# Performance work log

Hardware: AMD Instinct MI355X
Metric: run time of the kernel (lower is better)

The kernel has to match this reference:

```python
import jax, jax.numpy as jnp
import numpy as np

B, A, D = 512, 32, 256      # batch clips, actors (nodes per graph), feature dim
E = 1048576                 # total edges over the flattened (B*A)-node graph
THRESHOLD = 0.5             # config.knn.threshold
EPS = 1e-5


def setup_inputs() -> dict:
    key = jax.random.key(0)
    k1, k2, k3 = jax.random.split(key, 3)
    N = B * A
    X = jax.random.normal(k1, (B, A, D), dtype=jnp.float32)
    edge_index = jax.random.randint(k2, (2, E), 0, N, dtype=jnp.int32)
    W = jax.random.normal(k3, (D, D), dtype=jnp.float32) * (1.0 / np.sqrt(D))
    b = jnp.zeros((D,), dtype=jnp.float32)
    return {"X": X, "edge_index": edge_index, "W": W, "b": b}


def gcn_conv(x, edge_index, W, b):
    # Standard GCNConv: x' = D^-1/2 (A + I) D^-1/2 (x W) + b
    N = x.shape[0]
    x = x @ W                                            # [N, D]
    loop = jnp.arange(N, dtype=edge_index.dtype)
    src = jnp.concatenate([edge_index[0], loop])         # message sources
    tgt = jnp.concatenate([edge_index[1], loop])         # aggregation targets
    deg = jax.ops.segment_sum(jnp.ones_like(src, dtype=x.dtype), tgt,
                              num_segments=N)            # in-degree incl. self-loop
    dinv = jnp.where(deg > 0, jax.lax.rsqrt(deg), 0.0)
    coef = (dinv[src] * dinv[tgt])[:, None]              # symmetric norm per edge
    out = jax.ops.segment_sum(x[src] * coef, tgt, num_segments=N)
    return out + b


def reference(X, edge_index, W, b):
    Bq, Aq, Dq = X.shape
    x = X.reshape(Bq * Aq, Dq)
    x = gcn_conv(x, edge_index, W, b)
    Xo = x.reshape(Bq, Aq, Dq)

    # cal_edge: pairwise squared distances per batch, min-max normalized,
    # thresholded. Instead of variable-length dense_to_sparse edge lists we
    # return the equivalent fixed-shape adjacency mask [B, A, A].
    inner = -2.0 * jnp.einsum('bad,bcd->bac', Xo, Xo)
    sq = jnp.sum(Xo * Xo, axis=-1, keepdims=True)        # [B, A, 1]
    scores = sq + inner + jnp.swapaxes(sq, -1, -2)       # [B, A, A]
    smin = scores.min(axis=-1, keepdims=True)
    smax = scores.max(axis=-1, keepdims=True)
    scores = (scores - smin) / (smax - smin + EPS)
    adj_mask = scores > THRESHOLD                        # new edge set (dense form)
    return Xo, adj_mask
```

## Files before the change

### kernel.cpp

```cpp
#include <hip/hip_runtime.h>

#define BQ 512
#define AQ 32
#define DQ 256
#define NQ (BQ * AQ)
#define EQ 1048576
#define THR 0.5f
#define EPSF 1e-5f
#define DEG_STRIDE 160
#define BIN_TGTS 64
#define NBINS (NQ / BIN_TGTS)
#define BIN_STRIDE 4864

typedef __attribute__((ext_vector_type(8))) short bf16x8;
typedef __attribute__((ext_vector_type(4))) float f32x4;

__device__ __forceinline__ unsigned short f2bf(float f) {
    unsigned int u = __float_as_uint(f);
    return (unsigned short)((u + 0x7FFFu + ((u >> 16) & 1u)) >> 16);
}
__device__ __forceinline__ float bf2f(unsigned short h) {
    return __uint_as_float((unsigned int)h << 16);
}

__global__ __launch_bounds__(256) void k_prep_part(
        const float* __restrict__ W, unsigned short* __restrict__ Wt,
        const int* __restrict__ src, const int* __restrict__ tgt,
        int* __restrict__ bin_cursor, unsigned int* __restrict__ binned) {
    __shared__ int hist[NBINS];
    int tid = threadIdx.x;
    if (blockIdx.x < 256) {
        int idx = blockIdx.x * 256 + tid;
        int n = idx >> 8;
        int k = idx & 255;
        float w = W[k * DQ + n];
        unsigned short h = f2bf(w);
        Wt[idx] = h;
        Wt[DQ * DQ + idx] = f2bf(w - bf2f(h));
        return;
    }
    hist[tid] = 0;
    __syncthreads();
    int base = (blockIdx.x - 256) * 4096;
    int t[16], s[16];
    #pragma unroll
    for (int i = 0; i < 16; i++) {
        int e = base + i * 256 + tid;
        t[i] = tgt[e];
        s[i] = src[e];
        atomicAdd(&hist[t[i] >> 6], 1);
    }
    __syncthreads();
    int mine = hist[tid];
    __syncthreads();
    hist[tid] = tid * BIN_STRIDE + atomicAdd(&bin_cursor[tid], mine);
    __syncthreads();
    #pragma unroll
    for (int i = 0; i < 16; i++) {
        int slot = atomicAdd(&hist[t[i] >> 6], 1);
        binned[slot] = ((unsigned int)t[i] << 14) | (unsigned int)s[i];
    }
}

__global__ __launch_bounds__(256) void k_bucket_gemm(
        const float* __restrict__ Xp, const unsigned short* __restrict__ Wt,
        unsigned short* __restrict__ xwb,
        const int* __restrict__ bin_cursor, const unsigned int* __restrict__ binned,
        unsigned short* __restrict__ bucket, int* __restrict__ cnt,
        float* __restrict__ dinv) {
    __shared__ unsigned short lbuck[BIN_TGTS * DEG_STRIDE];
    __shared__ int lcnt[BIN_TGTS];
    int tid = threadIdx.x;
    if (blockIdx.x < NBINS) {
        int b = blockIdx.x;
        if (tid < BIN_TGTS) lcnt[tid] = 0;
        __syncthreads();
        int beg = b * BIN_STRIDE;
        int count = bin_cursor[b];
        if (count > BIN_STRIDE) count = BIN_STRIDE;
        int end = beg + count;
        for (int i = beg + tid; i < end; i += 256) {
            unsigned int ed = binned[i];
            int tl = (int)(ed >> 14) & 63;
            int pos = atomicAdd(&lcnt[tl], 1);
            if (pos < DEG_STRIDE)
                lbuck[tl * DEG_STRIDE + pos] = (unsigned short)(ed & 0x3FFFu);
        }
        __syncthreads();
        const unsigned int* lb32 = (const unsigned int*)lbuck;
        unsigned int* gb32 = (unsigned int*)(bucket + (size_t)b * BIN_TGTS * DEG_STRIDE);
        #pragma unroll
        for (int i = 0; i < 20; i++) gb32[i * 256 + tid] = lb32[i * 256 + tid];
        if (tid < BIN_TGTS) {
            int c = lcnt[tid];
            cnt[b * BIN_TGTS + tid] = c;
            dinv[b * BIN_TGTS + tid] = rsqrtf((float)(c + 1));
        }
        return;
    }
    int wave = tid >> 6;
    int lane = tid & 63;
    int col = lane & 15;
    int quad = lane >> 4;
    int mbase = (blockIdx.x - NBINS) * 64 + wave * 16;
    int m = mbase + col;

    const float* arow = Xp + (size_t)m * DQ;
    const unsigned short* Wlo = Wt + DQ * DQ;

    f32x4 acc[16];
    f32x4 zero = {0.f, 0.f, 0.f, 0.f};
    #pragma unroll
    for (int i = 0; i < 16; i++) acc[i] = zero;

    for (int k0 = 0; k0 < DQ; k0 += 32) {
        int kq = k0 + quad * 8;
        float4 a0 = *(const float4*)(arow + kq);
        float4 a1 = *(const float4*)(arow + kq + 4);
        float av[8] = {a0.x, a0.y, a0.z, a0.w, a1.x, a1.y, a1.z, a1.w};
        bf16x8 ah, al;
        #pragma unroll
        for (int j = 0; j < 8; j++) {
            unsigned short h = f2bf(av[j]);
            ah[j] = (short)h;
            al[j] = (short)f2bf(av[j] - bf2f(h));
        }
        #pragma unroll
        for (int nt = 0; nt < 16; nt++) {
            size_t boff = (size_t)(nt * 16 + col) * DQ + kq;
            bf16x8 bh = *(const bf16x8*)(Wt + boff);
            bf16x8 bl = *(const bf16x8*)(Wlo + boff);
            acc[nt] = __builtin_amdgcn_mfma_f32_16x16x32_bf16(ah, bh, acc[nt], 0, 0, 0);
            acc[nt] = __builtin_amdgcn_mfma_f32_16x16x32_bf16(al, bh, acc[nt], 0, 0, 0);
            acc[nt] = __builtin_amdgcn_mfma_f32_16x16x32_bf16(ah, bl, acc[nt], 0, 0, 0);
        }
    }

    #pragma unroll
    for (int nt = 0; nt < 16; nt++) {
        #pragma unroll
        for (int r = 0; r < 4; r++) {
            xwb[(size_t)(mbase + quad * 4 + r) * DQ + nt * 16 + col] =
                f2bf(acc[nt][r]);
        }
    }
}

__global__ __launch_bounds__(256) void k_agg(const unsigned int* __restrict__ xwb,
                                             const int* __restrict__ cnt,
                                             const unsigned short* __restrict__ bucket,
                                             const float* __restrict__ dinv,
                                             const float* __restrict__ bias,
                                             float* __restrict__ out) {
    int wave = threadIdx.x >> 6;
    int lane = threadIdx.x & 63;
    int t = blockIdx.x * 4 + wave;
    const uint2* xw2 = (const uint2*)xwb;

    float dt = dinv[t];
    float c0 = dt * dt;
    uint2 sp = xw2[(size_t)t * 64 + lane];
    float4 acc;
    acc.x = __uint_as_float(sp.x << 16) * c0;
    acc.y = __uint_as_float(sp.x & 0xFFFF0000u) * c0;
    acc.z = __uint_as_float(sp.y << 16) * c0;
    acc.w = __uint_as_float(sp.y & 0xFFFF0000u) * c0;

    const unsigned short* brow = bucket + t * DEG_STRIDE;
    int num = cnt[t];
    if (num > DEG_STRIDE) num = DEG_STRIDE;
    for (int k0 = 0; k0 < num; k0 += 64) {
        int rem = num - k0;
        int n = rem < 64 ? rem : 64;
        int idx = k0 + (lane < n ? lane : 0);
        int e = (int)brow[idx];
        float cl = (lane < n) ? dinv[e] * dt : 0.f;
        int n8 = (n + 7) & ~7;
        for (int j0 = 0; j0 < n8; j0 += 8) {
            #pragma unroll
            for (int jj = 0; jj < 8; jj++) {
                int j = j0 + jj;
                int s = __shfl(e, j);
                float c = __shfl(cl, j);
                uint2 p = xw2[(size_t)s * 64 + lane];
                acc.x += __uint_as_float(p.x << 16) * c;
                acc.y += __uint_as_float(p.x & 0xFFFF0000u) * c;
                acc.z += __uint_as_float(p.y << 16) * c;
                acc.w += __uint_as_float(p.y & 0xFFFF0000u) * c;
            }
        }
    }

    float4 bv = ((const float4*)bias)[lane];
    acc.x += bv.x; acc.y += bv.y; acc.z += bv.z; acc.w += bv.w;
    ((float4*)out)[(size_t)t * 64 + lane] = acc;
}

__global__ __launch_bounds__(256) void k_scores(const float* __restrict__ xo,
                                                float* __restrict__ mask) {
    __shared__ float xs[AQ][DQ + 4];
    __shared__ float sq[AQ];
    __shared__ float sc[AQ][AQ + 1];
    __shared__ float rmin[AQ], rmax[AQ];

    int bq = blockIdx.x;
    int tid = threadIdx.x;
    const float* xb = xo + (size_t)bq * AQ * DQ;

    #pragma unroll
    for (int k = 0; k < 8; k++) {
        int fidx = k * 256 + tid;
        float4 v = ((const float4*)xb)[fidx];
        *(float4*)&xs[fidx >> 6][(fidx & 63) * 4] = v;
    }
    __syncthreads();

    if (tid < AQ) {
        const float4* xi = (const float4*)xs[tid];
        float s = 0.f;
        #pragma unroll 8
        for (int dd = 0; dd < DQ / 4; dd++) {
            float4 a = xi[dd];
            s += a.x * a.x + a.y * a.y + a.z * a.z + a.w * a.w;
        }
        sq[tid] = s;
    }
    __syncthreads();

    {
        int p0 = tid * 4;
        int i = p0 >> 5;
        int j0 = p0 & 31;
        const float4* xi = (const float4*)xs[i];
        float g[4] = {0.f, 0.f, 0.f, 0.f};
        for (int dd = 0; dd < DQ / 4; dd += 8) {
            float4 ar[8];
            #pragma unroll
            for (int u = 0; u < 8; u++) ar[u] = xi[dd + u];
            #pragma unroll
            for (int q = 0; q < 4; q++) {
                const float4* xj = (const float4*)xs[j0 + q];
                float gq = 0.f;
                #pragma unroll
                for (int u = 0; u < 8; u++) {
                    float4 b = xj[dd + u];
                    gq += ar[u].x * b.x + ar[u].y * b.y +
                          ar[u].z * b.z + ar[u].w * b.w;
                }
                g[q] += gq;
            }
        }
        #pragma unroll
        for (int q = 0; q < 4; q++) {
            sc[i][j0 + q] = sq[i] - 2.f * g[q] + sq[j0 + q];
        }
    }
    __syncthreads();

    if (tid < AQ) {
        float mn = sc[tid][0], mx = sc[tid][0];
        for (int j = 1; j < AQ; j++) {
            float v = sc[tid][j];
            mn = fminf(mn, v);
            mx = fmaxf(mx, v);
        }
        rmin[tid] = mn;
        rmax[tid] = mx;
    }
    __syncthreads();

    float* mb = mask + (size_t)bq * AQ * AQ;
    {
        int p0 = tid * 4;
        int i = p0 >> 5, j0 = p0 & 31;
        float inv = 1.0f / (rmax[i] - rmin[i] + EPSF);
        float4 mv;
        mv.x = ((sc[i][j0 + 0] - rmin[i]) * inv > THR) ? 1.0f : 0.0f;
        mv.y = ((sc[i][j0 + 1] - rmin[i]) * inv > THR) ? 1.0f : 0.0f;
        mv.z = ((sc[i][j0 + 2] - rmin[i]) * inv > THR) ? 1.0f : 0.0f;
        mv.w = ((sc[i][j0 + 3] - rmin[i]) * inv > THR) ? 1.0f : 0.0f;
        ((float4*)mb)[tid] = mv;
    }
}

extern "C" void kernel_launch(void* const* d_in, const int* in_sizes, int n_in,
                              void* d_out, int out_size, void* d_ws, size_t ws_size,
                              hipStream_t stream) {
    const float* X    = (const float*)d_in[0];
    const int*   ei   = (const int*)d_in[1];
    const float* W    = (const float*)d_in[2];
    const float* bias = (const float*)d_in[3];
    float* out = (float*)d_out;

    char* ws = (char*)d_ws;
    unsigned short* xwb = (unsigned short*)ws;
    unsigned short* bucket = (unsigned short*)(ws + (size_t)NQ * DQ * 2);
    unsigned int* binned = (unsigned int*)(bucket + (size_t)NQ * DEG_STRIDE);
    unsigned short* Wt = (unsigned short*)(binned + (size_t)NBINS * BIN_STRIDE);
    int* cnt = (int*)(Wt + 2 * DQ * DQ);
    float* dinv = (float*)(cnt + NQ);
    int* bin_cursor = (int*)(dinv + NQ);

    const int* src = ei;
    const int* tgt = ei + EQ;

    hipMemsetAsync(bin_cursor, 0, NBINS * sizeof(int), stream);
    k_prep_part<<<512, 256, 0, stream>>>(W, Wt, src, tgt, bin_cursor, binned);
    k_bucket_gemm<<<512, 256, 0, stream>>>(X, Wt, xwb, bin_cursor, binned,
                                           bucket, cnt, dinv);
    k_agg<<<NQ / 4, 256, 0, stream>>>((const unsigned int*)xwb, cnt, bucket,
                                      dinv, bias, out);
    k_scores<<<BQ, 256, 0, stream>>>(out, out + (size_t)NQ * DQ);
}
```

Before: 190.3 us.

## Fuse edge aggregation and pairwise score kernels into one per-batch block

Merges the aggregation kernel and the score/mask kernel into a single launch with one 512-thread block per batch clip. Each of the 8 waves aggregates 4 actors and writes the result both to global output and directly into shared memory, so the score stage no longer re-reads the output from global memory and one launch is removed. The trade-off is fewer, larger blocks (512 instead of 4096 blocks for aggregation), which reduces the parallelism available to hide the latency of the irregular gather loads.

```diff
diff --git a/kernel.cpp b/kernel.cpp
--- a/kernel.cpp
+++ b/kernel.cpp
@@ -146,72 +146,68 @@
     }
 }
 
-__global__ __launch_bounds__(256) void k_agg(const unsigned int* __restrict__ xwb,
-                                             const int* __restrict__ cnt,
-                                             const unsigned short* __restrict__ bucket,
-                                             const float* __restrict__ dinv,
-                                             const float* __restrict__ bias,
-                                             float* __restrict__ out) {
-    int wave = threadIdx.x >> 6;
-    int lane = threadIdx.x & 63;
-    int t = blockIdx.x * 4 + wave;
-    const uint2* xw2 = (const uint2*)xwb;
-
-    float dt = dinv[t];
-    float c0 = dt * dt;
-    uint2 sp = xw2[(size_t)t * 64 + lane];
-    float4 acc;
-    acc.x = __uint_as_float(sp.x << 16) * c0;
-    acc.y = __uint_as_float(sp.x & 0xFFFF0000u) * c0;
-    acc.z = __uint_as_float(sp.y << 16) * c0;
-    acc.w = __uint_as_float(sp.y & 0xFFFF0000u) * c0;
-
-    const unsigned short* brow = bucket + t * DEG_STRIDE;
-    int num = cnt[t];
-    if (num > DEG_STRIDE) num = DEG_STRIDE;
-    for (int k0 = 0; k0 < num; k0 += 64) {
-        int rem = num - k0;
-        int n = rem < 64 ? rem : 64;
-        int idx = k0 + (lane < n ? lane : 0);
-        int e = (int)brow[idx];
-        float cl = (lane < n) ? dinv[e] * dt : 0.f;
-        int n8 = (n + 7) & ~7;
-        for (int j0 = 0; j0 < n8; j0 += 8) {
-            #pragma unroll
-            for (int jj = 0; jj < 8; jj++) {
-                int j = j0 + jj;
-                int s = __shfl(e, j);
-                float c = __shfl(cl, j);
-                uint2 p = xw2[(size_t)s * 64 + lane];
-                acc.x += __uint_as_float(p.x << 16) * c;
-                acc.y += __uint_as_float(p.x & 0xFFFF0000u) * c;
-                acc.z += __uint_as_float(p.y << 16) * c;
-                acc.w += __uint_as_float(p.y & 0xFFFF0000u) * c;
-            }
-        }
-    }
-
-    float4 bv = ((const float4*)bias)[lane];
-    acc.x += bv.x; acc.y += bv.y; acc.z += bv.z; acc.w += bv.w;
-    ((float4*)out)[(size_t)t * 64 + lane] = acc;
-}
-
-__global__ __launch_bounds__(256) void k_scores(const float* __restrict__ xo,
-                                                float* __restrict__ mask) {
+__global__ __launch_bounds__(512) void k_agg_scores(
+        const unsigned int* __restrict__ xwb,
+        const int* __restrict__ cnt,
+        const unsigned short* __restrict__ bucket,
+        const float* __restrict__ dinv,
+        const float* __restrict__ bias,
+        float* __restrict__ out,
+        float* __restrict__ mask) {
     __shared__ float xs[AQ][DQ + 4];
     __shared__ float sq[AQ];
     __shared__ float sc[AQ][AQ + 1];
     __shared__ float rmin[AQ], rmax[AQ];
 
+    int tid = threadIdx.x;
+    int wave = tid >> 6;
+    int lane = tid & 63;
     int bq = blockIdx.x;
-    int tid = threadIdx.x;
-    const float* xb = xo + (size_t)bq * AQ * DQ;
-
-    #pragma unroll
-    for (int k = 0; k < 8; k++) {
-        int fidx = k * 256 + tid;
-        float4 v = ((const float4*)xb)[fidx];
-        *(float4*)&xs[fidx >> 6][(fidx & 63) * 4] = v;
+    const uint2* xw2 = (const uint2*)xwb;
+
+    float4 bv = ((const float4*)bias)[lane];
+
+    #pragma unroll 1
+    for (int i = 0; i < 4; i++) {
+        int a = wave * 4 + i;
+        int t = bq * AQ + a;
+        float dt = dinv[t];
+        float c0 = dt * dt;
+        uint2 sp = xw2[(size_t)t * 64 + lane];
+        float4 acc;
+        acc.x = __uint_as_float(sp.x << 16) * c0;
+        acc.y = __uint_as_float(sp.x & 0xFFFF0000u) * c0;
+        acc.z = __uint_as_float(sp.y << 16) * c0;
+        acc.w = __uint_as_float(sp.y & 0xFFFF0000u) * c0;
+
+        const unsigned short* brow = bucket + t * DEG_STRIDE;
+        int num = cnt[t];
+        if (num > DEG_STRIDE) num = DEG_STRIDE;
+        for (int k0 = 0; k0 < num; k0 += 64) {
+            int rem = num - k0;
+            int n = rem < 64 ? rem : 64;
+            int idx = k0 + (lane < n ? lane : 0);
+            int e = (int)brow[idx];
+            float cl = (lane < n) ? dinv[e] * dt : 0.f;
+            int n8 = (n + 7) & ~7;
+            for (int j0 = 0; j0 < n8; j0 += 8) {
+                #pragma unroll
+                for (int jj = 0; jj < 8; jj++) {
+                    int j = j0 + jj;
+                    int s = __shfl(e, j);
+                    float c = __shfl(cl, j);
+                    uint2 p = xw2[(size_t)s * 64 + lane];
+                    acc.x += __uint_as_float(p.x << 16) * c;
+                    acc.y += __uint_as_float(p.x & 0xFFFF0000u) * c;
+                    acc.z += __uint_as_float(p.y << 16) * c;
+                    acc.w += __uint_as_float(p.y & 0xFFFF0000u) * c;
+                }
+            }
+        }
+
+        acc.x += bv.x; acc.y += bv.y; acc.z += bv.z; acc.w += bv.w;
+        ((float4*)out)[(size_t)t * 64 + lane] = acc;
+        *(float4*)&xs[a][lane * 4] = acc;
     }
     __syncthreads();
 
@@ -228,17 +224,17 @@
     __syncthreads();
 
     {
-        int p0 = tid * 4;
+        int p0 = tid * 2;
         int i = p0 >> 5;
         int j0 = p0 & 31;
         const float4* xi = (const float4*)xs[i];
-        float g[4] = {0.f, 0.f, 0.f, 0.f};
+        float g[2] = {0.f, 0.f};
         for (int dd = 0; dd < DQ / 4; dd += 8) {
             float4 ar[8];
             #pragma unroll
             for (int u = 0; u < 8; u++) ar[u] = xi[dd + u];
             #pragma unroll
-            for (int q = 0; q < 4; q++) {
+            for (int q = 0; q < 2; q++) {
                 const float4* xj = (const float4*)xs[j0 + q];
                 float gq = 0.f;
                 #pragma unroll
@@ -251,7 +247,7 @@
             }
         }
         #pragma unroll
-        for (int q = 0; q < 4; q++) {
+        for (int q = 0; q < 2; q++) {
             sc[i][j0 + q] = sq[i] - 2.f * g[q] + sq[j0 + q];
         }
     }
@@ -269,17 +265,15 @@
     }
     __syncthreads();
 
-    float* mb = mask + (size_t)bq * AQ * AQ;
     {
-        int p0 = tid * 4;
+        float* mb = mask + (size_t)bq * AQ * AQ;
+        int p0 = tid * 2;
         int i = p0 >> 5, j0 = p0 & 31;
         float inv = 1.0f / (rmax[i] - rmin[i] + EPSF);
-        float4 mv;
+        float2 mv;
         mv.x = ((sc[i][j0 + 0] - rmin[i]) * inv > THR) ? 1.0f : 0.0f;
         mv.y = ((sc[i][j0 + 1] - rmin[i]) * inv > THR) ? 1.0f : 0.0f;
-        mv.z = ((sc[i][j0 + 2] - rmin[i]) * inv > THR) ? 1.0f : 0.0f;
-        mv.w = ((sc[i][j0 + 3] - rmin[i]) * inv > THR) ? 1.0f : 0.0f;
-        ((float4*)mb)[tid] = mv;
+        ((float2*)mb)[tid] = mv;
     }
 }
 
@@ -308,7 +302,7 @@
     k_prep_part<<<512, 256, 0, stream>>>(W, Wt, src, tgt, bin_cursor, binned);
     k_bucket_gemm<<<512, 256, 0, stream>>>(X, Wt, xwb, bin_cursor, binned,
                                            bucket, cnt, dinv);
-    k_agg<<<NQ / 4, 256, 0, stream>>>((const unsigned int*)xwb, cnt, bucket,
-                                      dinv, bias, out);
-    k_scores<<<BQ, 256, 0, stream>>>(out, out + (size_t)NQ * DQ);
-}
+    k_agg_scores<<<BQ, 512, 0, stream>>>((const unsigned int*)xwb, cnt, bucket,
+                                         dinv, bias, out,
+                                         out + (size_t)NQ * DQ);
+}
```

New measurement: 186.7 us. Within noise of the previous version (-1.9%).
